# Kernel tuning notes

Measured on AMD Instinct MI355X. Metric: run time of the kernel, lower is better.

Reference implementation:

```python
import jax, jax.numpy as jnp
import numpy as np

# db1 (Haar) analysis lowpass is [1/sqrt2, 1/sqrt2]; 2D separable LL kernel is
# all-ones 2x2 * 0.5 with stride 2. With 'zero' mode and even H,W there is no
# boundary contribution, so DWT LL == 2x2 block sum * 0.5.
# Inverse with all high-freq bands zeroed: each output pixel = LL * 0.5
# (1/sqrt2 per spatial dim), i.e. nearest-neighbor upsample of LL*0.5.

def _haar_ll(x):
    # x: [B, C, H, W] -> [B, C, H/2, W/2]
    B, C, H, W = x.shape
    return x.reshape(B, C, H // 2, 2, W // 2, 2).sum(axis=(3, 5)) * 0.5

def _haar_inv_ll(ll):
    # ll: [B, C, H, W] -> [B, C, 2H, 2W], details assumed zero
    B, C, H, W = ll.shape
    y = (ll * 0.5)[:, :, :, None, :, None]
    return jnp.broadcast_to(y, (B, C, H, 2, W, 2)).reshape(B, C, 2 * H, 2 * W)

def setup_inputs() -> dict:
    key = jax.random.key(0)
    image = jax.random.normal(key, (32768, 1, 28, 28), dtype=jnp.float32)
    return {"image": image, "lev": 2}

def reference(image, lev):
    # Batched equivalent of: per-sample DWTForward(J=lev, db1, zero) -> zero Yh
    # -> DWTInverse. lev is a static Python int.
    x = image
    for _ in range(lev):
        x = _haar_ll(x)
    for _ in range(lev):
        x = _haar_inv_ll(x)
    return x
```

## Files before the change

kernel.cpp:

```cpp
#include <hip/hip_runtime.h>


typedef float f4 __attribute__((ext_vector_type(4)));

__global__ __launch_bounds__(256) void haar_ll2_nt(
    const float* __restrict__ in, float* __restrict__ out, int half) {
    int t = blockIdx.x * 256 + threadIdx.x;
    if (t >= half) return;

    const f4* __restrict__ in4  = reinterpret_cast<const f4*>(in);
    f4*       __restrict__ out4 = reinterpret_cast<f4*>(out);

    int p0, p1;
    {
        int b = t;
        int img = b / 49, rem = b - img * 49;
        int rg = rem / 7, cg = rem - rg * 7;
        p0 = img * 196 + rg * 28 + cg;
    }
    {
        int b = t + half;
        int img = b / 49, rem = b - img * 49;
        int rg = rem / 7, cg = rem - rg * 7;
        p1 = img * 196 + rg * 28 + cg;
    }

    f4 a0 = __builtin_nontemporal_load(in4 + p0);
    f4 b0 = __builtin_nontemporal_load(in4 + p0 + 7);
    f4 c0 = __builtin_nontemporal_load(in4 + p0 + 14);
    f4 d0 = __builtin_nontemporal_load(in4 + p0 + 21);
    f4 a1 = __builtin_nontemporal_load(in4 + p1);
    f4 b1 = __builtin_nontemporal_load(in4 + p1 + 7);
    f4 c1 = __builtin_nontemporal_load(in4 + p1 + 14);
    f4 d1 = __builtin_nontemporal_load(in4 + p1 + 21);

    float s0 = ((a0.x + a0.y) + (a0.z + a0.w)) + ((b0.x + b0.y) + (b0.z + b0.w)) +
               ((c0.x + c0.y) + (c0.z + c0.w)) + ((d0.x + d0.y) + (d0.z + d0.w));
    float s1 = ((a1.x + a1.y) + (a1.z + a1.w)) + ((b1.x + b1.y) + (b1.z + b1.w)) +
               ((c1.x + c1.y) + (c1.z + c1.w)) + ((d1.x + d1.y) + (d1.z + d1.w));
    s0 *= 0.0625f;
    s1 *= 0.0625f;

    f4 v0 = {s0, s0, s0, s0};
    f4 v1 = {s1, s1, s1, s1};
    __builtin_nontemporal_store(v0, out4 + p0);
    __builtin_nontemporal_store(v0, out4 + p0 + 7);
    __builtin_nontemporal_store(v0, out4 + p0 + 14);
    __builtin_nontemporal_store(v0, out4 + p0 + 21);
    __builtin_nontemporal_store(v1, out4 + p1);
    __builtin_nontemporal_store(v1, out4 + p1 + 7);
    __builtin_nontemporal_store(v1, out4 + p1 + 14);
    __builtin_nontemporal_store(v1, out4 + p1 + 21);
}

extern "C" void kernel_launch(void* const* d_in, const int* in_sizes, int n_in,
                              void* d_out, int out_size, void* d_ws, size_t ws_size,
                              hipStream_t stream) {
    const float* in  = (const float*)d_in[0];
    float*       out = (float*)d_out;
    int total = in_sizes[0] / 16;
    int half  = total / 2;
    int nblocks = (half + 255) / 256;
    haar_ll2_nt<<<nblocks, 256, 0, stream>>>(in, out, half);
}
```

Measured before the change: 181.7 us.

## Split Haar LL into reduce kernel and contiguous broadcast-store kernel

```diff
diff --git a/kernel.cpp b/kernel.cpp
--- a/kernel.cpp
+++ b/kernel.cpp
@@ -3,54 +3,55 @@
 
 typedef float f4 __attribute__((ext_vector_type(4)));
 
-__global__ __launch_bounds__(256) void haar_ll2_nt(
-    const float* __restrict__ in, float* __restrict__ out, int half) {
+__global__ __launch_bounds__(256) void haar_ll2_reduce(
+    const float* __restrict__ in, float* __restrict__ ll, int half) {
     int t = blockIdx.x * 256 + threadIdx.x;
     if (t >= half) return;
+    const f4* __restrict__ in4 = reinterpret_cast<const f4*>(in);
 
-    const f4* __restrict__ in4  = reinterpret_cast<const f4*>(in);
-    f4*       __restrict__ out4 = reinterpret_cast<f4*>(out);
-
-    int p0, p1;
-    {
-        int b = t;
-        int img = b / 49, rem = b - img * 49;
-        int rg = rem / 7, cg = rem - rg * 7;
-        p0 = img * 196 + rg * 28 + cg;
-    }
-    {
-        int b = t + half;
-        int img = b / 49, rem = b - img * 49;
-        int rg = rem / 7, cg = rem - rg * 7;
-        p1 = img * 196 + rg * 28 + cg;
-    }
+    int b0 = t, b1 = t + half;
+    int img0 = b0 / 49, rem0 = b0 - img0 * 49;
+    int rg0 = rem0 / 7,  cg0 = rem0 - rg0 * 7;
+    int p0 = img0 * 196 + rg0 * 28 + cg0;
+    int img1 = b1 / 49, rem1 = b1 - img1 * 49;
+    int rg1 = rem1 / 7,  cg1 = rem1 - rg1 * 7;
+    int p1 = img1 * 196 + rg1 * 28 + cg1;
 
     f4 a0 = __builtin_nontemporal_load(in4 + p0);
-    f4 b0 = __builtin_nontemporal_load(in4 + p0 + 7);
+    f4 b0v = __builtin_nontemporal_load(in4 + p0 + 7);
     f4 c0 = __builtin_nontemporal_load(in4 + p0 + 14);
     f4 d0 = __builtin_nontemporal_load(in4 + p0 + 21);
     f4 a1 = __builtin_nontemporal_load(in4 + p1);
-    f4 b1 = __builtin_nontemporal_load(in4 + p1 + 7);
+    f4 b1v = __builtin_nontemporal_load(in4 + p1 + 7);
     f4 c1 = __builtin_nontemporal_load(in4 + p1 + 14);
     f4 d1 = __builtin_nontemporal_load(in4 + p1 + 21);
 
-    float s0 = ((a0.x + a0.y) + (a0.z + a0.w)) + ((b0.x + b0.y) + (b0.z + b0.w)) +
+    float s0 = ((a0.x + a0.y) + (a0.z + a0.w)) + ((b0v.x + b0v.y) + (b0v.z + b0v.w)) +
                ((c0.x + c0.y) + (c0.z + c0.w)) + ((d0.x + d0.y) + (d0.z + d0.w));
-    float s1 = ((a1.x + a1.y) + (a1.z + a1.w)) + ((b1.x + b1.y) + (b1.z + b1.w)) +
+    float s1 = ((a1.x + a1.y) + (a1.z + a1.w)) + ((b1v.x + b1v.y) + (b1v.z + b1v.w)) +
                ((c1.x + c1.y) + (c1.z + c1.w)) + ((d1.x + d1.y) + (d1.z + d1.w));
-    s0 *= 0.0625f;
-    s1 *= 0.0625f;
+    ll[b0] = s0 * 0.0625f;
+    ll[b1] = s1 * 0.0625f;
+}
+
+__global__ __launch_bounds__(256) void haar_ll2_bcast(
+    const float* __restrict__ ll, float* __restrict__ out, int half) {
+    int t = blockIdx.x * 256 + threadIdx.x;
+    if (t >= half) return;
+    f4* __restrict__ out4 = reinterpret_cast<f4*>(out);
+
+    int f0 = t, f1 = t + half;
+    int img0 = f0 / 196, rem0 = f0 - img0 * 196;
+    int r0 = rem0 / 7,   cg0 = rem0 - r0 * 7;
+    float s0 = ll[img0 * 49 + (r0 >> 2) * 7 + cg0];
+    int img1 = f1 / 196, rem1 = f1 - img1 * 196;
+    int r1 = rem1 / 7,   cg1 = rem1 - r1 * 7;
+    float s1 = ll[img1 * 49 + (r1 >> 2) * 7 + cg1];
 
     f4 v0 = {s0, s0, s0, s0};
     f4 v1 = {s1, s1, s1, s1};
-    __builtin_nontemporal_store(v0, out4 + p0);
-    __builtin_nontemporal_store(v0, out4 + p0 + 7);
-    __builtin_nontemporal_store(v0, out4 + p0 + 14);
-    __builtin_nontemporal_store(v0, out4 + p0 + 21);
-    __builtin_nontemporal_store(v1, out4 + p1);
-    __builtin_nontemporal_store(v1, out4 + p1 + 7);
-    __builtin_nontemporal_store(v1, out4 + p1 + 14);
-    __builtin_nontemporal_store(v1, out4 + p1 + 21);
+    __builtin_nontemporal_store(v0, out4 + f0);
+    __builtin_nontemporal_store(v1, out4 + f1);
 }
 
 extern "C" void kernel_launch(void* const* d_in, const int* in_sizes, int n_in,
@@ -58,8 +59,13 @@
                               hipStream_t stream) {
     const float* in  = (const float*)d_in[0];
     float*       out = (float*)d_out;
-    int total = in_sizes[0] / 16;
-    int half  = total / 2;
-    int nblocks = (half + 255) / 256;
-    haar_ll2_nt<<<nblocks, 256, 0, stream>>>(in, out, half);
+    float*       ll  = (float*)d_ws;
+
+    int total_blocks = in_sizes[0] / 16;
+    int h1 = total_blocks / 2;
+    haar_ll2_reduce<<<(h1 + 255) / 256, 256, 0, stream>>>(in, ll, h1);
+
+    int total_f4 = in_sizes[0] / 4;
+    int h2 = total_f4 / 2;
+    haar_ll2_bcast<<<(h2 + 255) / 256, 256, 0, stream>>>(ll, out, h2);
 }
```

New measurement: 176.8 us. 2.7% less time.
